# Optimization experiments

Measured on AMD Instinct MI355X. Metric: run time of the kernel, lower is better.

Reference implementation:

```python
import jax, jax.numpy as jnp
import numpy as np

N, E, D, H, G, L, EF = 50000, 800000, 128, 256, 512, 3, 8
BN_EPS = 1e-5


def _bn(h, g, b):
    # torch BatchNorm1d in training mode: biased batch stats over the node axis
    m = h.mean(0)
    v = h.var(0)
    return g * (h - m) * jax.lax.rsqrt(v + BN_EPS) + b


def setup_inputs() -> dict:
    ks = jax.random.split(jax.random.key(0), 12)
    sc = 0.05
    return {
        "x": jax.random.normal(ks[0], (N, D), jnp.float32),
        "edge_attr": jax.random.normal(ks[1], (E, EF), jnp.float32),
        "vn_emb": jnp.zeros((1, D), jnp.float32),  # init.constant_(0)
        "We": jax.random.normal(ks[2], (L, EF, D)) * sc,
        "be": jnp.zeros((L, D)),
        "W1": jax.random.normal(ks[3], (L, D, H)) * sc,
        "b1": jnp.zeros((L, H)),
        "g1": jnp.ones((L, H)),
        "bt1": jnp.zeros((L, H)),
        "W2": jax.random.normal(ks[4], (L, H, D)) * sc,
        "b2": jnp.zeros((L, D)),
        "gb": jnp.ones((L, D)),
        "bb": jnp.zeros((L, D)),
        "Wv1": jax.random.normal(ks[5], (L - 1, D, H)) * sc,
        "bv1": jnp.zeros((L - 1, H)),
        "gv1": jnp.ones((L - 1, H)),
        "btv1": jnp.zeros((L - 1, H)),
        "Wv2": jax.random.normal(ks[6], (L - 1, H, D)) * sc,
        "bv2": jnp.zeros((L - 1, D)),
        "gv2": jnp.ones((L - 1, D)),
        "btv2": jnp.zeros((L - 1, D)),
        "edge_index": jax.random.randint(ks[7], (2, E), 0, N),
        "batch": jnp.sort(jax.random.randint(ks[8], (N,), 0, G)),
    }


def reference(x, edge_attr, vn_emb, We, be, W1, b1, g1, bt1, W2, b2, gb, bb,
              Wv1, bv1, gv1, btv1, Wv2, bv2, gv2, btv2, edge_index, batch):
    src, dst = edge_index[0], edge_index[1]
    vn = jnp.broadcast_to(vn_emb, (G, D))  # Embedding(1, D) looked up for every graph
    h = x  # node_encoder is None -> encoded_node = x
    for l in range(L):
        h_in = h + vn[batch]                              # virtual-node broadcast (gather)
        e = edge_attr @ We[l] + be[l]                     # per-layer edge encoder
        msg = jax.nn.relu(h_in[src] + e)                  # GIN message, [E, D]
        aggr = jax.ops.segment_sum(msg, dst, num_segments=N)
        z = h_in + aggr                                   # (1+eps)*h + aggr, eps=0
        z = jax.nn.relu(_bn(z @ W1[l] + b1[l], g1[l], bt1[l]))
        h = _bn(z @ W2[l] + b2[l], gb[l], bb[l])          # conv MLP out + outer BatchNorm
        if l < L - 1:
            h = jax.nn.relu(h)                            # dropout ratio 0 -> identity
            pooled = jax.ops.segment_sum(h_in, batch, num_segments=G) + vn
            t = jax.nn.relu(_bn(pooled @ Wv1[l] + bv1[l], gv1[l], btv1[l]))
            vn = jax.nn.relu(_bn(t @ Wv2[l] + bv2[l], gv2[l], btv2[l]))
    return h  # JK == 'last'
```

## Files before the change

kernel.cpp:

```cpp
#include <hip/hip_runtime.h>
#include <hip/hip_bf16.h>

#define N_NODES 50000
#define N_EDGES 800000
#define DIM 128
#define HID 256
#define N_GRAPH 512
#define N_LAYER 3
#define EFEAT 8
#define BN_EPS 1e-5f

typedef unsigned short u16;
typedef unsigned int u32;

using bf16x8_t = short __attribute__((ext_vector_type(8)));
using f32x4_t  = float __attribute__((ext_vector_type(4)));
using f32x2    = float __attribute__((ext_vector_type(2)));
using f32x4v   = float __attribute__((ext_vector_type(4)));


__device__ __forceinline__ void atomic_add_f(float* p, float v) {
    unsafeAtomicAdd(p, v);
}
__device__ __forceinline__ u16 f2bf(float x) {
    union { float f; u32 u; } v; v.f = x;
    u32 r = v.u + 0x7FFF + ((v.u >> 16) & 1);
    return (u16)(r >> 16);
}
__device__ __forceinline__ float bf2f(u16 u) {
    union { u32 i; float f; } v; v.i = (u32)u << 16; return v.f;
}
__device__ __forceinline__ float2 up2(u32 p) {
    return make_float2(bf2f((u16)(p & 0xFFFF)), bf2f((u16)(p >> 16)));
}
__device__ __forceinline__ u32 pk2(float a, float b) {
    return (u32)f2bf(a) | ((u32)f2bf(b) << 16);
}
__device__ __forceinline__ float bflo(u32 u) {
    union { u32 i; float f; } v; v.i = u << 16; return v.f;
}
__device__ __forceinline__ float bfhi(u32 u) {
    union { u32 i; float f; } v; v.i = u & 0xFFFF0000u; return v.f;
}
__device__ __forceinline__ f32x2 up2p(u32 p) {
    union { u32 u[2]; f32x2 f; } v;
    v.u[0] = p << 16;
    v.u[1] = p & 0xFFFF0000u;
    return v.f;
}
__device__ __forceinline__ f32x2 splat2(float x) {
    f32x2 r; r.x = x; r.y = x; return r;
}

__global__ __launch_bounds__(256) void wconv_kernel(
    const float* __restrict__ W1, const float* __restrict__ W2,
    u16* __restrict__ W1t, u16* __restrict__ W2t)
{
    int idx = blockIdx.x * 256 + threadIdx.x;
    if (idx >= 6 * 32768) return;
    int m = idx >> 15;
    int off = idx & 32767;
    int l = m >> 1;
    if ((m & 1) == 0) {
        int r = off >> 8, c = off & 255;
        W1t[(size_t)l * 32768 + c * 128 + r] = f2bf(W1[(size_t)l * 32768 + r * 256 + c]);
    } else {
        int r = off >> 7, c = off & 127;
        W2t[(size_t)l * 32768 + c * 256 + r] = f2bf(W2[(size_t)l * 32768 + r * 128 + c]);
    }
}

__global__ __launch_bounds__(256) void hist_rank_kernel(
    const int* __restrict__ ei, int* __restrict__ deg, int* __restrict__ rank)
{
    int e = blockIdx.x * 256 + threadIdx.x;
    if (e >= N_EDGES) return;
    int dst = ei[N_EDGES + e];
    rank[e] = atomicAdd(&deg[dst], 1);
}

__global__ __launch_bounds__(1024) void scan_kernel(const int* __restrict__ deg, int* __restrict__ rowptr) {
    __shared__ int wsum[16];
    __shared__ int carry;
    int tid = threadIdx.x;
    if (tid == 0) { carry = 0; rowptr[0] = 0; }
    __syncthreads();
    for (int base = 0; base < N_NODES; base += 1024) {
        int i = base + tid;
        int v = (i < N_NODES) ? deg[i] : 0;
        int lane = tid & 63, w = tid >> 6;
        int s = v;
        #pragma unroll
        for (int d = 1; d < 64; d <<= 1) { int t = __shfl_up(s, d); if (lane >= d) s += t; }
        if (lane == 63) wsum[w] = s;
        __syncthreads();
        if (tid < 64) {
            int t = (tid < 16) ? wsum[tid] : 0;
            #pragma unroll
            for (int d = 1; d < 16; d <<= 1) { int u = __shfl_up(t, d); if (tid >= d) t += u; }
            if (tid < 16) wsum[tid] = t;
        }
        __syncthreads();
        int excl = (w > 0) ? wsum[w - 1] : 0;
        int incl = s + excl + carry;
        if (i < N_NODES) rowptr[i + 1] = incl;
        __syncthreads();
        if (tid == 0) carry += wsum[15];
        __syncthreads();
    }
}

__global__ __launch_bounds__(256) void scatter_kernel(
    const int* __restrict__ ei, const float* __restrict__ ea,
    const int* __restrict__ rank, const int* __restrict__ rowptr,
    char* __restrict__ rec)
{
    int e = blockIdx.x * 256 + threadIdx.x;
    if (e >= N_EDGES) return;
    int src = __builtin_nontemporal_load(ei + e);
    int dst = __builtin_nontemporal_load(ei + N_EDGES + e);
    int rk  = __builtin_nontemporal_load(rank + e);
    int pos = rowptr[dst] + rk;
    f32x4v lo = __builtin_nontemporal_load((const f32x4v*)(ea + (size_t)e * EFEAT));
    f32x4v hi = __builtin_nontemporal_load((const f32x4v*)(ea + (size_t)e * EFEAT + 4));
    uint4 q;
    q.x = pk2(lo.x, lo.y); q.y = pk2(lo.z, lo.w);
    q.z = pk2(hi.x, hi.y); q.w = pk2(hi.z, hi.w);
    char* rb = rec + ((size_t)pos << 5);
    *(uint4*)rb = q;
    *(u32*)(rb + 16) = (u32)src << 8;
}

template <bool USEBN, int VNM>
__global__ __launch_bounds__(256) void hin_kernel(
    const float* __restrict__ src,
    const float* __restrict__ sum2, const float* __restrict__ ss2,
    const float* __restrict__ g, const float* __restrict__ b, float invN,
    const int* __restrict__ batch,
    const float* __restrict__ vn_emb,
    const float* __restrict__ vnpre, const float* __restrict__ vsum, const float* __restrict__ vss,
    const float* __restrict__ gv, const float* __restrict__ btv, float invG,
    u16* __restrict__ hin, int total4)
{
    int idx = blockIdx.x * 256 + threadIdx.x;
    if (idx >= total4) return;
    int base = idx * 4;
    int n = base >> 7;
    int c = base & (DIM - 1);
    float4 v = *(const float4*)(src + base);
    float o[4] = {v.x, v.y, v.z, v.w};
    if (USEBN) {
        #pragma unroll
        for (int j = 0; j < 4; ++j) {
            int cj = c + j;
            float m = sum2[cj] * invN;
            float var = ss2[cj] * invN - m * m;
            float r = rsqrtf(var + BN_EPS);
            float a = g[cj] * r;
            o[j] = fmaxf(fmaf(a, o[j], b[cj] - m * a), 0.f);
        }
    }
    int grp = batch[n];
    if (VNM == 0) {
        const float4 w = *(const float4*)(vn_emb + c);
        o[0] += w.x; o[1] += w.y; o[2] += w.z; o[3] += w.w;
    } else {
        const float4 vp = *(const float4*)(vnpre + (size_t)grp * DIM + c);
        float vv[4] = {vp.x, vp.y, vp.z, vp.w};
        #pragma unroll
        for (int j = 0; j < 4; ++j) {
            int cj = c + j;
            float m = vsum[cj] * invG;
            float var = vss[cj] * invG - m * m;
            float r = rsqrtf(var + BN_EPS);
            float a = gv[cj] * r;
            o[j] += fmaxf(fmaf(a, vv[j], btv[cj] - m * a), 0.f);
        }
    }
    uint2 pk;
    pk.x = pk2(o[0], o[1]);
    pk.y = pk2(o[2], o[3]);
    *(uint2*)(hin + base) = pk;
}

__device__ __forceinline__ void edge_term2(
    u32 h, uint4 eq, const f32x2* rW, f32x2 rB, f32x2& acc)
{
    f32x2 ex = rB;
    ex = __builtin_elementwise_fma(splat2(bflo(eq.x)), rW[0], ex);
    ex = __builtin_elementwise_fma(splat2(bfhi(eq.x)), rW[1], ex);
    ex = __builtin_elementwise_fma(splat2(bflo(eq.y)), rW[2], ex);
    ex = __builtin_elementwise_fma(splat2(bfhi(eq.y)), rW[3], ex);
    ex = __builtin_elementwise_fma(splat2(bflo(eq.z)), rW[4], ex);
    ex = __builtin_elementwise_fma(splat2(bfhi(eq.z)), rW[5], ex);
    ex = __builtin_elementwise_fma(splat2(bflo(eq.w)), rW[6], ex);
    ex = __builtin_elementwise_fma(splat2(bfhi(eq.w)), rW[7], ex);
    f32x2 s = up2p(h) + ex;
    s = __builtin_elementwise_max(s, splat2(0.f));
    acc += s;
}

__global__ __launch_bounds__(256) void aggr_kernel(
    const int* __restrict__ rowptr, const char* __restrict__ rec,
    const float* __restrict__ Wel, const float* __restrict__ bel,
    const u16* __restrict__ hin, u16* __restrict__ z, int nWaves)
{
    const int lane = threadIdx.x & 63;
    const int cb = lane * 4;
    const int wid0 = (blockIdx.x << 2) + (threadIdx.x >> 6);

    f32x2 rW[EFEAT];
    #pragma unroll
    for (int k = 0; k < EFEAT; ++k) {
        float2 t = *(const float2*)(Wel + k * DIM + lane * 2);
        rW[k].x = t.x; rW[k].y = t.y;
    }
    float2 tb = *(const float2*)(bel + lane * 2);
    f32x2 rB; rB.x = tb.x; rB.y = tb.y;

    const char* hinB = (const char*)hin;

    for (int node = __builtin_amdgcn_readfirstlane(wid0); node < N_NODES; node += nWaves) {
        int beg = rowptr[node];
        int end = rowptr[node + 1];
        f32x2 acc = up2p(*(const u32*)(hinB + ((u32)node << 8) + cb));

        const char* rb = rec + ((size_t)beg << 5);
        int i = beg;
        for (; i + 3 < end; i += 4, rb += 128) {
            uint4 e0 = *(const uint4*)(rb);
            u32  s0 = *(const u32*)(rb + 16);
            uint4 e1 = *(const uint4*)(rb + 32);
            u32  s1 = *(const u32*)(rb + 48);
            uint4 e2 = *(const uint4*)(rb + 64);
            u32  s2 = *(const u32*)(rb + 80);
            uint4 e3 = *(const uint4*)(rb + 96);
            u32  s3 = *(const u32*)(rb + 112);
            u32 h0 = *(const u32*)(hinB + s0 + cb);
            u32 h1 = *(const u32*)(hinB + s1 + cb);
            u32 h2 = *(const u32*)(hinB + s2 + cb);
            u32 h3 = *(const u32*)(hinB + s3 + cb);
            edge_term2(h0, e0, rW, rB, acc);
            edge_term2(h1, e1, rW, rB, acc);
            edge_term2(h2, e2, rW, rB, acc);
            edge_term2(h3, e3, rW, rB, acc);
        }
        for (; i < end; ++i, rb += 32) {
            uint4 e0 = *(const uint4*)(rb);
            u32  s0 = *(const u32*)(rb + 16);
            u32 h0 = *(const u32*)(hinB + s0 + cb);
            edge_term2(h0, e0, rW, rB, acc);
        }
        *(u32*)(z + ((size_t)node << 7) + lane * 2) = pk2(acc.x, acc.y);
    }
}

template <int MODE, bool CBF16>
__global__ __launch_bounds__(256) void gemm_bf16_kernel(
    const u16* __restrict__ Aa,
    const float* __restrict__ sSum, const float* __restrict__ sSS,
    const float* __restrict__ gA, const float* __restrict__ btA, float invCnt,
    const u16* __restrict__ Bt,
    const float* __restrict__ bias,
    void* __restrict__ CoutV,
    float* __restrict__ outSum, float* __restrict__ outSS,
    int M, int K, int Nc)
{
    constexpr int BM = 128, BN = 128, BK = 128;
    constexpr int LDA = BK + 8;
    __shared__ u16 As[BM * LDA];
    __shared__ u16 Bs[64 * LDA];
    __shared__ float csum[BN], css[BN];

    const int tid = threadIdx.x;
    const int wave = tid >> 6, lane = tid & 63;
    const int row0 = blockIdx.x * BM, col0 = blockIdx.y * BN;
    const int w_m = (wave & 1) * 64, w_n = (wave >> 1) * 32;
    const int quad = lane >> 4, l16 = lane & 15;

    if (tid < BN) { csum[tid] = 0.f; css[tid] = 0.f; }

    f32x4_t acc[4][4];
    #pragma unroll
    for (int mi = 0; mi < 4; ++mi)
        #pragma unroll
        for (int ni = 0; ni < 4; ++ni)
            acc[mi][ni] = (f32x4_t){0.f, 0.f, 0.f, 0.f};

    const int kc = (tid & 15) * 8;
    const int nkt = K / BK;

    for (int kt = 0; kt < nkt; ++kt) {
        float af[8], bf_[8];
        if (MODE == 1) {
            #pragma unroll
            for (int j = 0; j < 8; ++j) {
                int kg = kt * BK + kc + j;
                float m = sSum[kg] * invCnt;
                float var = sSS[kg] * invCnt - m * m;
                float r = rsqrtf(var + BN_EPS);
                float a = gA[kg] * r;
                af[j] = a;
                bf_[j] = btA[kg] - m * a;
            }
        }
        #pragma unroll
        for (int it = 0; it < 8; ++it) {
            int chunk = it * 256 + tid;
            int row = chunk >> 4;
            int gr = row0 + row; if (gr >= M) gr = M - 1;
            uint4 q = *(const uint4*)(Aa + (size_t)gr * K + kt * BK + kc);
            if (MODE == 1) {
                float2 p0 = up2(q.x), p1 = up2(q.y), p2 = up2(q.z), p3 = up2(q.w);
                p0.x = fmaxf(fmaf(af[0], p0.x, bf_[0]), 0.f);
                p0.y = fmaxf(fmaf(af[1], p0.y, bf_[1]), 0.f);
                p1.x = fmaxf(fmaf(af[2], p1.x, bf_[2]), 0.f);
                p1.y = fmaxf(fmaf(af[3], p1.y, bf_[3]), 0.f);
                p2.x = fmaxf(fmaf(af[4], p2.x, bf_[4]), 0.f);
                p2.y = fmaxf(fmaf(af[5], p2.y, bf_[5]), 0.f);
                p3.x = fmaxf(fmaf(af[6], p3.x, bf_[6]), 0.f);
                p3.y = fmaxf(fmaf(af[7], p3.y, bf_[7]), 0.f);
                q.x = pk2(p0.x, p0.y); q.y = pk2(p1.x, p1.y);
                q.z = pk2(p2.x, p2.y); q.w = pk2(p3.x, p3.y);
            }
            *(uint4*)(As + row * LDA + kc) = q;
        }
        #pragma unroll
        for (int half = 0; half < 2; ++half) {
            #pragma unroll
            for (int it = 0; it < 4; ++it) {
                int chunk = it * 256 + tid;
                int n = chunk >> 4;
                uint4 q = *(const uint4*)(Bt + (size_t)(col0 + half * 64 + n) * K + kt * BK + kc);
                *(uint4*)(Bs + n * LDA + kc) = q;
            }
            __syncthreads();
            #pragma unroll
            for (int ks = 0; ks < 4; ++ks) {
                bf16x8_t a_frag[4], b_frag[2];
                #pragma unroll
                for (int mi = 0; mi < 4; ++mi)
                    a_frag[mi] = *(const bf16x8_t*)(As + (w_m + mi * 16 + l16) * LDA + ks * 32 + quad * 8);
                #pragma unroll
                for (int ni = 0; ni < 2; ++ni)
                    b_frag[ni] = *(const bf16x8_t*)(Bs + (w_n + ni * 16 + l16) * LDA + ks * 32 + quad * 8);
                #pragma unroll
                for (int mi = 0; mi < 4; ++mi)
                    #pragma unroll
                    for (int ni = 0; ni < 2; ++ni)
                        acc[mi][half * 2 + ni] = __builtin_amdgcn_mfma_f32_16x16x32_bf16(
                            a_frag[mi], b_frag[ni], acc[mi][half * 2 + ni], 0, 0, 0);
            }
            __syncthreads();
        }
    }

    u16* Cb = (u16*)CoutV;
    float* Cf = (float*)CoutV;
    #pragma unroll
    for (int half = 0; half < 2; ++half)
    #pragma unroll
    for (int ni = 0; ni < 2; ++ni) {
        int ccol = half * 64 + w_n + ni * 16 + l16;
        int col = col0 + ccol;
        float bv = bias[col];
        float s = 0.f, qs = 0.f;
        #pragma unroll
        for (int mi = 0; mi < 4; ++mi) {
            int rbase = row0 + w_m + mi * 16 + quad * 4;
            #pragma unroll
            for (int reg = 0; reg < 4; ++reg) {
                int gr = rbase + reg;
                if (gr < M) {
                    float o = acc[mi][half * 2 + ni][reg] + bv;
                    s += o;
                    qs += o * o;
                    if (CBF16) Cb[(size_t)gr * Nc + col] = f2bf(o);
                    else       Cf[(size_t)gr * Nc + col] = o;
                }
            }
        }
        s += __shfl_xor(s, 16);  s += __shfl_xor(s, 32);
        qs += __shfl_xor(qs, 16);  qs += __shfl_xor(qs, 32);
        if (quad == 0) {
            atomicAdd(&csum[ccol], s);
            atomicAdd(&css[ccol], qs);
        }
    }
    __syncthreads();
    if (tid < BN) {
        atomic_add_f(outSum + col0 + tid, csum[tid]);
        atomic_add_f(outSS + col0 + tid, css[tid]);
    }
}

template <int MODE>
__global__ __launch_bounds__(256) void gemm_kernel(
    const float* __restrict__ Aa,
    const float* __restrict__ sSum, const float* __restrict__ sSS,
    const float* __restrict__ gA, const float* __restrict__ btA, float invCnt,
    const float* __restrict__ B, const float* __restrict__ bias,
    float* __restrict__ Cout, float* __restrict__ outSum, float* __restrict__ outSS,
    int M, int K, int Nc)
{
    __shared__ float As[16][68];
    __shared__ float Bs[16][64];
    __shared__ float alphaS[256], betaS[256];
    __shared__ float csum[64], css[64];

    const int tid = threadIdx.x;
    const int tx = tid & 15, ty = tid >> 4;
    const int row0 = blockIdx.x * 64, col0 = blockIdx.y * 64;

    if (tid < 64) { csum[tid] = 0.f; css[tid] = 0.f; }
    if (MODE == 1) {
        for (int k = tid; k < K; k += 256) {
            float m = sSum[k] * invCnt;
            float var = sSS[k] * invCnt - m * m;
            float r = rsqrtf(var + BN_EPS);
            float a = gA[k] * r;
            alphaS[k] = a;
            betaS[k] = btA[k] - m * a;
        }
    }
    __syncthreads();

    float acc[4][4];
    #pragma unroll
    for (int i = 0; i < 4; ++i)
        #pragma unroll
        for (int j = 0; j < 4; ++j) acc[i][j] = 0.f;

    const int lr = tid >> 2;
    const int lk = (tid & 3) * 4;
    const int bk = tid >> 4;
    const int bc = tx * 4;

    for (int kt = 0; kt < K; kt += 16) {
        int gr = row0 + lr;
        float4 va = make_float4(0.f, 0.f, 0.f, 0.f);
        if (gr < M) {
            va = *(const float4*)(Aa + (size_t)gr * K + kt + lk);
            if (MODE == 1) {
                int k0 = kt + lk;
                va.x = fmaxf(fmaf(alphaS[k0 + 0], va.x, betaS[k0 + 0]), 0.f);
                va.y = fmaxf(fmaf(alphaS[k0 + 1], va.y, betaS[k0 + 1]), 0.f);
                va.z = fmaxf(fmaf(alphaS[k0 + 2], va.z, betaS[k0 + 2]), 0.f);
                va.w = fmaxf(fmaf(alphaS[k0 + 3], va.w, betaS[k0 + 3]), 0.f);
            }
        }
        As[lk + 0][lr] = va.x;
        As[lk + 1][lr] = va.y;
        As[lk + 2][lr] = va.z;
        As[lk + 3][lr] = va.w;
        const float4 vb4 = *(const float4*)(B + (size_t)(kt + bk) * Nc + col0 + bc);
        *(float4*)&Bs[bk][bc] = vb4;
        __syncthreads();
        #pragma unroll
        for (int kk = 0; kk < 16; ++kk) {
            const float4 a4 = *(const float4*)&As[kk][ty * 4];
            const float4 b4 = *(const float4*)&Bs[kk][tx * 4];
            float av[4] = {a4.x, a4.y, a4.z, a4.w};
            float bv4[4] = {b4.x, b4.y, b4.z, b4.w};
            #pragma unroll
            for (int i = 0; i < 4; ++i)
                #pragma unroll
                for (int j = 0; j < 4; ++j)
                    acc[i][j] = fmaf(av[i], bv4[j], acc[i][j]);
        }
        __syncthreads();
    }

    const float4 bvv = *(const float4*)(bias + col0 + tx * 4);
    float bias4[4] = {bvv.x, bvv.y, bvv.z, bvv.w};
    float ps[4] = {0.f, 0.f, 0.f, 0.f};
    float pq[4] = {0.f, 0.f, 0.f, 0.f};
    #pragma unroll
    for (int i = 0; i < 4; ++i) {
        int gr = row0 + ty * 4 + i;
        if (gr < M) {
            float o[4];
            #pragma unroll
            for (int j = 0; j < 4; ++j) {
                o[j] = acc[i][j] + bias4[j];
                ps[j] += o[j];
                pq[j] += o[j] * o[j];
            }
            *(float4*)(Cout + (size_t)gr * Nc + col0 + tx * 4) = make_float4(o[0], o[1], o[2], o[3]);
        }
    }
    #pragma unroll
    for (int j = 0; j < 4; ++j) {
        atomicAdd(&csum[tx * 4 + j], ps[j]);
        atomicAdd(&css[tx * 4 + j], pq[j]);
    }
    __syncthreads();
    if (tid < 64) {
        atomic_add_f(outSum + col0 + tid, csum[tid]);
        atomic_add_f(outSS + col0 + tid, css[tid]);
    }
}

template <int VNM>
__global__ __launch_bounds__(128) void pooled_seg_kernel(
    const u16* __restrict__ hin, const int* __restrict__ batch,
    const float* __restrict__ vn_emb,
    const float* __restrict__ vnpre, const float* __restrict__ vsum, const float* __restrict__ vss,
    const float* __restrict__ gv, const float* __restrict__ btv, float invG,
    float* __restrict__ pooled)
{
    int g = blockIdx.x;
    int c = threadIdx.x;
    int lo = 0, hi = N_NODES;
    while (lo < hi) { int mid = (lo + hi) >> 1; if (batch[mid] < g) lo = mid + 1; else hi = mid; }
    int start = lo;
    hi = N_NODES;
    while (lo < hi) { int mid = (lo + hi) >> 1; if (batch[mid] < g + 1) lo = mid + 1; else hi = mid; }
    int end = lo;
    float acc;
    if (VNM == 0) {
        acc = vn_emb[c];
    } else {
        float m = vsum[c] * invG;
        float var = vss[c] * invG - m * m;
        float r = rsqrtf(var + BN_EPS);
        float a = gv[c] * r;
        acc = fmaxf(fmaf(a, vnpre[(size_t)g * DIM + c], btv[c] - m * a), 0.f);
    }
    float a0 = 0.f, a1 = 0.f, a2 = 0.f, a3 = 0.f;
    int n = start;
    for (; n + 3 < end; n += 4) {
        a0 += bf2f(hin[(size_t)(n + 0) * DIM + c]);
        a1 += bf2f(hin[(size_t)(n + 1) * DIM + c]);
        a2 += bf2f(hin[(size_t)(n + 2) * DIM + c]);
        a3 += bf2f(hin[(size_t)(n + 3) * DIM + c]);
    }
    for (; n < end; ++n) a0 += bf2f(hin[(size_t)n * DIM + c]);
    acc += (a0 + a1) + (a2 + a3);
    pooled[(size_t)g * DIM + c] = acc;
}

__global__ __launch_bounds__(256) void final_bn_kernel(
    float* __restrict__ outp, const float* __restrict__ sum2, const float* __restrict__ ss2,
    const float* __restrict__ g, const float* __restrict__ b, float invN, int total4)
{
    int idx = blockIdx.x * 256 + threadIdx.x;
    if (idx >= total4) return;
    int base = idx * 4;
    int c = base & (DIM - 1);
    float4 v = *(const float4*)(outp + base);
    float o[4] = {v.x, v.y, v.z, v.w};
    #pragma unroll
    for (int j = 0; j < 4; ++j) {
        int cj = c + j;
        float m = sum2[cj] * invN;
        float var = ss2[cj] * invN - m * m;
        float r = rsqrtf(var + BN_EPS);
        float a = g[cj] * r;
        o[j] = fmaf(a, o[j], b[cj] - m * a);
    }
    *(float4*)(outp + base) = make_float4(o[0], o[1], o[2], o[3]);
}

extern "C" void kernel_launch(void* const* d_in, const int* in_sizes, int n_in,
                              void* d_out, int out_size, void* d_ws, size_t ws_size,
                              hipStream_t stream) {
    const float* x         = (const float*)d_in[0];
    const float* edge_attr = (const float*)d_in[1];
    const float* vn_emb    = (const float*)d_in[2];
    const float* We        = (const float*)d_in[3];
    const float* be        = (const float*)d_in[4];
    const float* W1        = (const float*)d_in[5];
    const float* b1        = (const float*)d_in[6];
    const float* g1v       = (const float*)d_in[7];
    const float* bt1       = (const float*)d_in[8];
    const float* W2        = (const float*)d_in[9];
    const float* b2        = (const float*)d_in[10];
    const float* gb        = (const float*)d_in[11];
    const float* bb        = (const float*)d_in[12];
    const float* Wv1       = (const float*)d_in[13];
    const float* bv1       = (const float*)d_in[14];
    const float* gv1       = (const float*)d_in[15];
    const float* btv1      = (const float*)d_in[16];
    const float* Wv2       = (const float*)d_in[17];
    const float* bv2       = (const float*)d_in[18];
    const float* gv2       = (const float*)d_in[19];
    const float* btv2      = (const float*)d_in[20];
    const int* edge_index  = (const int*)d_in[21];
    const int* batch       = (const int*)d_in[22];
    float* outp = (float*)d_out;

    auto au = [](size_t x) { return (x + 255) & ~(size_t)255; };
    char* p = (char*)d_ws;
    u16* h_in   = (u16*)p;  p += au((size_t)N_NODES * DIM * 2);
    u16* z_bf   = (u16*)p;  p += au((size_t)N_NODES * DIM * 2);
    u16* c1_bf  = (u16*)p;  p += au((size_t)N_NODES * HID * 2);
    u16* W1t    = (u16*)p;  p += au((size_t)3 * 32768 * 2);
    u16* W2t    = (u16*)p;  p += au((size_t)3 * 32768 * 2);
    float* pooled = (float*)p;  p += au((size_t)N_GRAPH * DIM * 4);
    float* tpre   = (float*)p;  p += au((size_t)N_GRAPH * HID * 4);
    float* vnpre  = (float*)p;  p += au((size_t)N_GRAPH * DIM * 4);
    float* stats  = (float*)p;  p += au(2048 * 4);
    float* sum1 = stats,        *ss1 = stats + 256;
    float* sum2 = stats + 512,  *ss2 = stats + 640;
    float* vsum1 = stats + 768, *vss1 = stats + 1024;
    float* vsum2 = stats + 1280, *vss2 = stats + 1408;
    int* rowptr = (int*)p;  p += au((size_t)(N_NODES + 1) * 4);
    int* deg    = (int*)p;  p += au((size_t)N_NODES * 4);
    int* rank   = (int*)p;  p += au((size_t)N_EDGES * 4);
    char* rec   = p;

    const float invN = 1.0f / (float)N_NODES;
    const float invG = 1.0f / (float)N_GRAPH;
    const int total4 = N_NODES * DIM / 4;

    hipMemsetAsync(deg, 0, N_NODES * sizeof(int), stream);
    hist_rank_kernel<<<(N_EDGES + 255) / 256, 256, 0, stream>>>(edge_index, deg, rank);
    scan_kernel<<<1, 1024, 0, stream>>>(deg, rowptr);
    scatter_kernel<<<(N_EDGES + 255) / 256, 256, 0, stream>>>(
        edge_index, edge_attr, rank, rowptr, rec);
    wconv_kernel<<<768, 256, 0, stream>>>(W1, W2, W1t, W2t);

    const int AGGR_BLOCKS = 2048;
    const int nWaves = AGGR_BLOCKS * 4;

    for (int l = 0; l < N_LAYER; ++l) {
        if (l == 0)
            hin_kernel<false, 0><<<(total4 + 255) / 256, 256, 0, stream>>>(
                x, nullptr, nullptr, nullptr, nullptr, 0.f, batch,
                vn_emb, nullptr, nullptr, nullptr, nullptr, nullptr, 0.f,
                h_in, total4);
        else
            hin_kernel<true, 1><<<(total4 + 255) / 256, 256, 0, stream>>>(
                outp, sum2, ss2, gb + (size_t)(l - 1) * DIM, bb + (size_t)(l - 1) * DIM, invN, batch,
                nullptr, vnpre, vsum2, vss2,
                gv2 + (size_t)(l - 1) * DIM, btv2 + (size_t)(l - 1) * DIM, invG,
                h_in, total4);

        if (l == 0)
            pooled_seg_kernel<0><<<N_GRAPH, 128, 0, stream>>>(
                h_in, batch, vn_emb, nullptr, nullptr, nullptr, nullptr, nullptr, 0.f, pooled);
        else if (l < N_LAYER - 1)
            pooled_seg_kernel<1><<<N_GRAPH, 128, 0, stream>>>(
                h_in, batch, nullptr, vnpre, vsum2, vss2,
                gv2 + (size_t)(l - 1) * DIM, btv2 + (size_t)(l - 1) * DIM, invG, pooled);

        hipMemsetAsync(stats, 0, 2048 * sizeof(float), stream);

        aggr_kernel<<<AGGR_BLOCKS, 256, 0, stream>>>(
            rowptr, rec, We + (size_t)l * EFEAT * DIM, be + (size_t)l * DIM,
            h_in, z_bf, nWaves);

        dim3 g1d((N_NODES + 127) / 128, HID / 128);
        gemm_bf16_kernel<0, true><<<g1d, 256, 0, stream>>>(
            z_bf, nullptr, nullptr, nullptr, nullptr, 0.f,
            W1t + (size_t)l * 32768, b1 + (size_t)l * HID,
            (void*)c1_bf, sum1, ss1, N_NODES, DIM, HID);

        dim3 g2d((N_NODES + 127) / 128, DIM / 128);
        gemm_bf16_kernel<1, false><<<g2d, 256, 0, stream>>>(
            c1_bf, sum1, ss1, g1v + (size_t)l * HID, bt1 + (size_t)l * HID, invN,
            W2t + (size_t)l * 32768, b2 + (size_t)l * DIM,
            (void*)outp, sum2, ss2, N_NODES, HID, DIM);

        if (l < N_LAYER - 1) {
            dim3 g3d(N_GRAPH / 64, HID / 64);
            gemm_kernel<0><<<g3d, 256, 0, stream>>>(
                pooled, nullptr, nullptr, nullptr, nullptr, 0.f,
                Wv1 + (size_t)l * DIM * HID, bv1 + (size_t)l * HID,
                tpre, vsum1, vss1, N_GRAPH, DIM, HID);

            dim3 g4d(N_GRAPH / 64, DIM / 64);
            gemm_kernel<1><<<g4d, 256, 0, stream>>>(
                tpre, vsum1, vss1, gv1 + (size_t)l * HID, btv1 + (size_t)l * HID, invG,
                Wv2 + (size_t)l * HID * DIM, bv2 + (size_t)l * DIM,
                vnpre, vsum2, vss2, N_GRAPH, HID, DIM);
        }
    }

    final_bn_kernel<<<(total4 + 255) / 256, 256, 0, stream>>>(
        outp, sum2, ss2, gb + (size_t)2 * DIM, bb + (size_t)2 * DIM, invN, total4);
}
```

Before: 775.5 us.

## Pack CSR edges into padded groups of four with software-pipelined gather

Edge records are regrouped into 80-byte groups of four, with the four source offsets stored first and then the four bf16 edge-feature vectors. The scan now counts groups per node instead of edges. The aggregation loop prefetches the next group's source indices and node features while it computes the current group, so gather latency overlaps with math. The record buffer must be zeroed to pad partial groups, which adds a memset and some wasted bandwidth on padding, and the prefetch reads one group past the end of each node's range.

Result: no change. 779.1 us (+0.5%).

```diff
diff --git a/kernel.cpp b/kernel.cpp
--- a/kernel.cpp
+++ b/kernel.cpp
@@ -9,6 +9,7 @@
 #define N_LAYER 3
 #define EFEAT 8
 #define BN_EPS 1e-5f
+#define MAX_GROUPS 240000
 
 typedef unsigned short u16;
 typedef unsigned int u32;
@@ -79,15 +80,15 @@
     rank[e] = atomicAdd(&deg[dst], 1);
 }
 
-__global__ __launch_bounds__(1024) void scan_kernel(const int* __restrict__ deg, int* __restrict__ rowptr) {
+__global__ __launch_bounds__(1024) void scan_kernel(const int* __restrict__ deg, int* __restrict__ grpptr) {
     __shared__ int wsum[16];
     __shared__ int carry;
     int tid = threadIdx.x;
-    if (tid == 0) { carry = 0; rowptr[0] = 0; }
+    if (tid == 0) { carry = 0; grpptr[0] = 0; }
     __syncthreads();
     for (int base = 0; base < N_NODES; base += 1024) {
         int i = base + tid;
-        int v = (i < N_NODES) ? deg[i] : 0;
+        int v = (i < N_NODES) ? ((deg[i] + 3) >> 2) : 0;
         int lane = tid & 63, w = tid >> 6;
         int s = v;
         #pragma unroll
@@ -103,7 +104,7 @@
         __syncthreads();
         int excl = (w > 0) ? wsum[w - 1] : 0;
         int incl = s + excl + carry;
-        if (i < N_NODES) rowptr[i + 1] = incl;
+        if (i < N_NODES) grpptr[i + 1] = incl;
         __syncthreads();
         if (tid == 0) carry += wsum[15];
         __syncthreads();
@@ -112,7 +113,7 @@
 
 __global__ __launch_bounds__(256) void scatter_kernel(
     const int* __restrict__ ei, const float* __restrict__ ea,
-    const int* __restrict__ rank, const int* __restrict__ rowptr,
+    const int* __restrict__ rank, const int* __restrict__ grpptr,
     char* __restrict__ rec)
 {
     int e = blockIdx.x * 256 + threadIdx.x;
@@ -120,15 +121,16 @@
     int src = __builtin_nontemporal_load(ei + e);
     int dst = __builtin_nontemporal_load(ei + N_EDGES + e);
     int rk  = __builtin_nontemporal_load(rank + e);
-    int pos = rowptr[dst] + rk;
+    int grp = grpptr[dst] + (rk >> 2);
+    int j = rk & 3;
     f32x4v lo = __builtin_nontemporal_load((const f32x4v*)(ea + (size_t)e * EFEAT));
     f32x4v hi = __builtin_nontemporal_load((const f32x4v*)(ea + (size_t)e * EFEAT + 4));
     uint4 q;
     q.x = pk2(lo.x, lo.y); q.y = pk2(lo.z, lo.w);
     q.z = pk2(hi.x, hi.y); q.w = pk2(hi.z, hi.w);
-    char* rb = rec + ((size_t)pos << 5);
-    *(uint4*)rb = q;
-    *(u32*)(rb + 16) = (u32)src << 8;
+    char* rb = rec + (size_t)grp * 80;
+    *(uint4*)(rb + 16 + j * 16) = q;
+    *(u32*)(rb + j * 4) = (u32)src << 8;
 }
 
 template <bool USEBN, int VNM>
@@ -201,7 +203,8 @@
 }
 
 __global__ __launch_bounds__(256) void aggr_kernel(
-    const int* __restrict__ rowptr, const char* __restrict__ rec,
+    const int* __restrict__ grpptr, const int* __restrict__ deg,
+    const char* __restrict__ rec,
     const float* __restrict__ Wel, const float* __restrict__ bel,
     const u16* __restrict__ hin, u16* __restrict__ z, int nWaves)
 {
@@ -221,35 +224,50 @@
     const char* hinB = (const char*)hin;
 
     for (int node = __builtin_amdgcn_readfirstlane(wid0); node < N_NODES; node += nWaves) {
-        int beg = rowptr[node];
-        int end = rowptr[node + 1];
+        int g0 = grpptr[node];
+        int ng = grpptr[node + 1] - g0;
+        int dg = deg[node];
         f32x2 acc = up2p(*(const u32*)(hinB + ((u32)node << 8) + cb));
 
-        const char* rb = rec + ((size_t)beg << 5);
-        int i = beg;
-        for (; i + 3 < end; i += 4, rb += 128) {
-            uint4 e0 = *(const uint4*)(rb);
-            u32  s0 = *(const u32*)(rb + 16);
-            uint4 e1 = *(const uint4*)(rb + 32);
-            u32  s1 = *(const u32*)(rb + 48);
-            uint4 e2 = *(const uint4*)(rb + 64);
-            u32  s2 = *(const u32*)(rb + 80);
-            uint4 e3 = *(const uint4*)(rb + 96);
-            u32  s3 = *(const u32*)(rb + 112);
-            u32 h0 = *(const u32*)(hinB + s0 + cb);
-            u32 h1 = *(const u32*)(hinB + s1 + cb);
-            u32 h2 = *(const u32*)(hinB + s2 + cb);
-            u32 h3 = *(const u32*)(hinB + s3 + cb);
+        if (ng > 0) {
+            const char* base = rec + (size_t)g0 * 80;
+            uint4 so = *(const uint4*)base;
+            uint4 e0 = *(const uint4*)(base + 16);
+            uint4 e1 = *(const uint4*)(base + 32);
+            uint4 e2 = *(const uint4*)(base + 48);
+            uint4 e3 = *(const uint4*)(base + 64);
+            u32 h0 = *(const u32*)(hinB + so.x + cb);
+            u32 h1 = *(const u32*)(hinB + so.y + cb);
+            u32 h2 = *(const u32*)(hinB + so.z + cb);
+            u32 h3 = *(const u32*)(hinB + so.w + cb);
+            uint4 soA = *(const uint4*)(base + 80);
+            const char* pn = base + 80;
+
+            #pragma unroll 1
+            for (int c = 0; c < ng - 1; ++c) {
+                u32 i0 = *(const u32*)(hinB + soA.x + cb);
+                u32 i1 = *(const u32*)(hinB + soA.y + cb);
+                u32 i2 = *(const u32*)(hinB + soA.z + cb);
+                u32 i3 = *(const u32*)(hinB + soA.w + cb);
+                uint4 soN = *(const uint4*)(pn + 80);
+                uint4 f0 = *(const uint4*)(pn + 16);
+                uint4 f1 = *(const uint4*)(pn + 32);
+                uint4 f2 = *(const uint4*)(pn + 48);
+                uint4 f3 = *(const uint4*)(pn + 64);
+                edge_term2(h0, e0, rW, rB, acc);
+                edge_term2(h1, e1, rW, rB, acc);
+                edge_term2(h2, e2, rW, rB, acc);
+                edge_term2(h3, e3, rW, rB, acc);
+                h0 = i0; h1 = i1; h2 = i2; h3 = i3;
+                e0 = f0; e1 = f1; e2 = f2; e3 = f3;
+                soA = soN;
+                pn += 80;
+            }
+            int valid = dg - (ng - 1) * 4;
             edge_term2(h0, e0, rW, rB, acc);
-            edge_term2(h1, e1, rW, rB, acc);
-            edge_term2(h2, e2, rW, rB, acc);
-            edge_term2(h3, e3, rW, rB, acc);
-        }
-        for (; i < end; ++i, rb += 32) {
-            uint4 e0 = *(const uint4*)(rb);
-            u32  s0 = *(const u32*)(rb + 16);
-            u32 h0 = *(const u32*)(hinB + s0 + cb);
-            edge_term2(h0, e0, rW, rB, acc);
+            if (valid > 1) edge_term2(h1, e1, rW, rB, acc);
+            if (valid > 2) edge_term2(h2, e2, rW, rB, acc);
+            if (valid > 3) edge_term2(h3, e3, rW, rB, acc);
         }
         *(u32*)(z + ((size_t)node << 7) + lane * 2) = pk2(acc.x, acc.y);
     }
@@ -605,20 +623,22 @@
     float* sum2 = stats + 512,  *ss2 = stats + 640;
     float* vsum1 = stats + 768, *vss1 = stats + 1024;
     float* vsum2 = stats + 1280, *vss2 = stats + 1408;
-    int* rowptr = (int*)p;  p += au((size_t)(N_NODES + 1) * 4);
+    int* grpptr = (int*)p;  p += au((size_t)(N_NODES + 1) * 4);
     int* deg    = (int*)p;  p += au((size_t)N_NODES * 4);
     int* rank   = (int*)p;  p += au((size_t)N_EDGES * 4);
     char* rec   = p;
 
+    const size_t REC_BYTES = (size_t)MAX_GROUPS * 80 + 256;
     const float invN = 1.0f / (float)N_NODES;
     const float invG = 1.0f / (float)N_GRAPH;
     const int total4 = N_NODES * DIM / 4;
 
     hipMemsetAsync(deg, 0, N_NODES * sizeof(int), stream);
+    hipMemsetAsync(rec, 0, REC_BYTES, stream);
     hist_rank_kernel<<<(N_EDGES + 255) / 256, 256, 0, stream>>>(edge_index, deg, rank);
-    scan_kernel<<<1, 1024, 0, stream>>>(deg, rowptr);
+    scan_kernel<<<1, 1024, 0, stream>>>(deg, grpptr);
     scatter_kernel<<<(N_EDGES + 255) / 256, 256, 0, stream>>>(
-        edge_index, edge_attr, rank, rowptr, rec);
+        edge_index, edge_attr, rank, grpptr, rec);
     wconv_kernel<<<768, 256, 0, stream>>>(W1, W2, W1t, W2t);
 
     const int AGGR_BLOCKS = 2048;
@@ -648,7 +668,7 @@
         hipMemsetAsync(stats, 0, 2048 * sizeof(float), stream);
 
         aggr_kernel<<<AGGR_BLOCKS, 256, 0, stream>>>(
-            rowptr, rec, We + (size_t)l * EFEAT * DIM, be + (size_t)l * DIM,
+            grpptr, deg, rec, We + (size_t)l * EFEAT * DIM, be + (size_t)l * DIM,
             h_in, z_bf, nWaves);
 
         dim3 g1d((N_NODES + 127) / 128, HID / 128);
```
